# Optimization experiments

Measured on AMD Instinct MI355X. Metric: run time of the kernel, lower is better.

The kernel has to match this reference:

```python
import jax, jax.numpy as jnp
import numpy as np

NUM_RBF = 16
TOP_K = 30
MAX_REL = 32  # max_relative_feature
EPS_D = 1e-6
LN_EPS = 1e-5


def _rbf(D):
    # D: [..., ] -> [..., NUM_RBF]
    mu = jnp.linspace(2.0, 22.0, NUM_RBF)
    sigma = (22.0 - 2.0) / NUM_RBF
    return jnp.exp(-(((D[..., None] - mu) / sigma) ** 2))


def _gather_nb(coords, E_idx):
    # coords: [B,L,3], E_idx: [B,L,K] -> [B,L,K,3]
    return jax.vmap(lambda c, i: c[i])(coords, E_idx)


def reference(X, mask, residue_idx, chain_labels, pe_w, pe_b, edge_w, ln_g, ln_b):
    B, L = X.shape[0], X.shape[1]
    N = X[:, :, 0, :]
    C = X[:, :, 1, :]
    Ca = X[:, :, 2, :]
    O = X[:, :, 3, :]
    # virtual C-beta
    b = Ca - N
    c = C - Ca
    a = jnp.cross(b, c)
    Cb = -0.58273431 * a + 0.56802827 * b - 0.54067466 * c + Ca

    # kNN over masked pairwise C-C distances
    mask2 = mask[:, None, :] * mask[:, :, None]  # [B,L,L]
    dX = C[:, None, :, :] - C[:, :, None, :]
    D = mask2 * jnp.sqrt(jnp.sum(dX ** 2, -1) + EPS_D)
    D_max = jnp.max(D, -1, keepdims=True)
    D_adjust = D + (1.0 - mask2) * D_max
    k = min(TOP_K, L)
    neg_vals, E_idx = jax.lax.top_k(-D_adjust, k)  # smallest distances
    D_neighbors = -neg_vals  # [B,L,K]

    # 25 RBF feature sets: first is the masked topk distance, then 24 atom pairs
    atoms = {'N': N, 'C': C, 'Ca': Ca, 'Cb': Cb, 'O': O}
    pairs = [('N','N'),('Ca','Ca'),('Cb','Cb'),('C','N'),('C','Ca'),('C','Cb'),
             ('N','Ca'),('N','Cb'),('Cb','Ca'),('N','C'),('Ca','C'),('Cb','C'),
             ('Ca','N'),('Cb','N'),('Ca','Cb'),('O','O'),('C','O'),('O','C'),
             ('N','O'),('O','N'),('Cb','O'),('O','Ca'),('O','Cb'),('Ca','O')]
    A_stack = jnp.stack([atoms[p[0]] for p in pairs], 0)  # [P,B,L,3]
    B_stack = jnp.stack([atoms[p[1]] for p in pairs], 0)  # [P,B,L,3]
    Bn = jax.vmap(lambda cb: _gather_nb(cb, E_idx))(B_stack)  # [P,B,L,K,3]
    D_pairs = jnp.sqrt(jnp.sum((A_stack[:, :, :, None, :] - Bn) ** 2, -1) + EPS_D)  # [P,B,L,K]
    RBF_pairs = _rbf(D_pairs)  # [P,B,L,K,R]
    P = len(pairs)
    RBF_pairs = jnp.moveaxis(RBF_pairs, 0, 3).reshape(B, L, k, P * NUM_RBF)
    RBF_all = jnp.concatenate([_rbf(D_neighbors), RBF_pairs], -1)  # [B,L,K,400]

    # positional encodings (relative residue offset gathered at neighbors)
    offset = residue_idx[:, :, None] - residue_idx[:, None, :]  # [B,L,L]
    offset = jnp.take_along_axis(offset, E_idx, axis=2)  # [B,L,K]
    d_chains = (chain_labels[:, :, None] - chain_labels[:, None, :] == 0).astype(jnp.int32)
    E_chains = jnp.take_along_axis(d_chains, E_idx, axis=2)  # [B,L,K]
    d = jnp.clip(offset + MAX_REL, 0, 2 * MAX_REL) * E_chains + (1 - E_chains) * (2 * MAX_REL + 1)
    E_positional = pe_w[d] + pe_b  # one-hot @ W == row gather; [B,L,K,16]

    E = jnp.concatenate([E_positional, RBF_all], -1)  # [B,L,K,416]
    E = E @ edge_w  # [B,L,K,128]
    mu = jnp.mean(E, -1, keepdims=True)
    var = jnp.mean((E - mu) ** 2, -1, keepdims=True)
    E = (E - mu) / jnp.sqrt(var + LN_EPS) * ln_g + ln_b
    return E, E_idx


def setup_inputs() -> dict:
    key = jax.random.key(0)
    ks = jax.random.split(key, 6)
    B, L = 4, 2048
    X = jax.random.normal(ks[0], (B, L, 4, 3), dtype=jnp.float32)
    mask = jnp.ones((B, L), dtype=jnp.float32)
    residue_idx = jnp.arange(B * L, dtype=jnp.int32).reshape(B, L)
    chain_labels = jnp.zeros((B, L), dtype=jnp.int32)
    pe_w = jax.random.normal(ks[1], (66, 16), dtype=jnp.float32) * 0.1
    pe_b = jax.random.normal(ks[2], (16,), dtype=jnp.float32) * 0.1
    edge_w = jax.random.normal(ks[3], (416, 128), dtype=jnp.float32) * 0.05
    ln_g = jnp.ones((128,), dtype=jnp.float32)
    ln_b = jnp.zeros((128,), dtype=jnp.float32)
    return {"X": X, "mask": mask, "residue_idx": residue_idx, "chain_labels": chain_labels,
            "pe_w": pe_w, "pe_b": pe_b, "edge_w": edge_w, "ln_g": ln_g, "ln_b": ln_b}
```

## Files before the change

### kernel.cpp

```cpp
#include <hip/hip_runtime.h>
#include <hip/hip_bf16.h>
#include <cstdint>
#include <cstddef>

#define Bc 4
#define Lc 2048
#define Kc 30
#define Fc 416
#define Nc 128

typedef __bf16 bf16x8 __attribute__((ext_vector_type(8)));
typedef float  f32x4  __attribute__((ext_vector_type(4)));
typedef unsigned short ushortx8 __attribute__((ext_vector_type(8)));

__constant__ int c_pa[24] = {0,2,3,1,1,1,0,0,3,0,2,3,2,3,2,4,1,4,0,4,3,4,4,2};
__constant__ int c_pb[24] = {0,2,3,0,2,3,2,3,2,1,1,1,0,0,3,4,4,1,4,0,4,2,3,2};

__device__ __forceinline__ unsigned long long u64min(unsigned long long a, unsigned long long b) {
    return a < b ? a : b;
}
__device__ __forceinline__ unsigned long long u64max(unsigned long long a, unsigned long long b) {
    return a > b ? a : b;
}

__device__ __forceinline__ unsigned short f2bf(float f) {
    __hip_bfloat16 h = __float2bfloat16(f);
    return *(unsigned short*)&h;
}

__device__ __forceinline__ void rbf8(float d, float mu0, float* v) {
    const float u0 = (d - mu0) * 0.8f;
    v[0] = __expf(-u0 * u0);
    float rr = __expf(fmaf(2.1333333f, u0, -1.1377778f));
    #pragma unroll
    for (int m = 1; m < 8; ++m) {
        v[m] = v[m - 1] * rr;
        rr *= 0.10274083f;
    }
}

template<int CTRL>
__device__ __forceinline__ float dpp_radd(float x) {
    const int r = __builtin_amdgcn_update_dpp(0, __float_as_int(x), CTRL, 0xf, 0xf, true);
    return x + __int_as_float(r);
}
__device__ __forceinline__ float row16_sum(float x) {
    x = dpp_radd<0x121>(x);
    x = dpp_radd<0x122>(x);
    x = dpp_radd<0x124>(x);
    x = dpp_radd<0x128>(x);
    return x;
}

__global__ __launch_bounds__(256) void prep_all(const float* __restrict__ Wg,
                                                const float* __restrict__ X,
                                                const float* __restrict__ mask,
                                                unsigned short* __restrict__ Wt,
                                                float4* __restrict__ Cpk) {
    const int blk = blockIdx.x;
    if (blk < 208) {
        const int id = blk * 256 + threadIdx.x;
        const int n = id / Fc, k = id - n * Fc;
        Wt[id] = f2bf(Wg[k * Nc + n]);
    } else {
        const int id = (blk - 208) * 256 + threadIdx.x;
        float4 o;
        o.x = X[(size_t)id * 12 + 3];
        o.y = X[(size_t)id * 12 + 4];
        o.z = X[(size_t)id * 12 + 5];
        o.w = mask[id];
        Cpk[id] = o;
    }
}

__global__ __launch_bounds__(256) void topk3(
    const float4* __restrict__ Cpk,
    int* __restrict__ eidx, float* __restrict__ dnb, float* __restrict__ outEidx)
{
#pragma clang fp contract(off)
    __shared__ unsigned long long pairs[4][256];
    __shared__ int scnt[4];
    const int t = threadIdx.x;
    const int lane = t & 63, wv = t >> 6;
    const int row = blockIdx.x * 4 + wv;

    if (lane == 0) scnt[wv] = 0;

    const float4 ci = Cpk[row];
    const float cix = ci.x, ciy = ci.y, ciz = ci.z, mi = ci.w;
    const float4* base = Cpk + (row & ~(Lc - 1));

    float D[32], am[32];
    float dmax = -1e30f;
    #pragma unroll 8
    for (int s = 0; s < 32; ++s) {
        const float4 f4 = base[s * 64 + lane];
        const float dx = f4.x - cix;
        const float dy = f4.y - ciy;
        const float dz = f4.z - ciz;
        const float ss = dx * dx + dy * dy + dz * dz;
        const float dist = sqrtf(ss + 1e-6f);
        const float m2 = mi * f4.w;
        D[s] = m2 * dist;
        am[s] = 1.0f - m2;
        dmax = fmaxf(dmax, D[s]);
    }
    #pragma unroll
    for (int off = 32; off; off >>= 1) dmax = fmaxf(dmax, __shfl_xor(dmax, off, 64));

    unsigned uv[32];
    unsigned long long lmin = ~0ULL;
    #pragma unroll 8
    for (int s = 0; s < 32; ++s) {
        const float Dadj = D[s] + am[s] * dmax;
        uv[s] = __float_as_uint(Dadj);
        const unsigned long long k =
            ((unsigned long long)uv[s] << 32) | (unsigned)(s * 64 + lane);
        lmin = u64min(lmin, k);
    }

    unsigned long long sv = lmin;
    #pragma unroll
    for (int k = 2; k <= 64; k <<= 1) {
        #pragma unroll
        for (int j = k >> 1; j > 0; j >>= 1) {
            const unsigned long long o =
                (unsigned long long)__shfl_xor((long long)sv, j, 64);
            const bool takeMin = (((lane & k) == 0) == ((lane & j) == 0));
            sv = takeMin ? u64min(sv, o) : u64max(sv, o);
        }
    }
    const unsigned long long Tkey =
        (unsigned long long)__shfl((long long)sv, 29, 64);

    #pragma unroll 8
    for (int s = 0; s < 32; ++s) {
        const unsigned long long key =
            ((unsigned long long)uv[s] << 32) | (unsigned)(s * 64 + lane);
        if (key <= Tkey) {
            const int pos = atomicAdd(&scnt[wv], 1);
            if (pos < 256) pairs[wv][pos] = key;
        }
    }
    const int S = min(scnt[wv], 256);

    for (int p = lane; p < S; p += 64) {
        const unsigned long long kp = pairs[wv][p];
        int r = 0;
        for (int q = 0; q < S; ++q)
            r += (pairs[wv][q] < kp) ? 1 : 0;
        if (r < Kc) {
            const int j = (int)(kp & 0xffffffffULL);
            eidx[row * Kc + r] = j;
            dnb[row * Kc + r] = __uint_as_float((unsigned)(kp >> 32));
            outEidx[(size_t)row * Kc + r] = (float)j;
        }
    }
}

__global__ __launch_bounds__(512, 4) void edge_mfma5(
    const float* __restrict__ X, const int* __restrict__ ridx, const int* __restrict__ clab,
    const float* __restrict__ pe_w, const float* __restrict__ pe_b,
    const unsigned short* __restrict__ Wt,
    const float* __restrict__ ln_g, const float* __restrict__ ln_b,
    const int* __restrict__ eidx, const float* __restrict__ dnb,
    float* __restrict__ outE)
{
    __shared__ unsigned short Bs[2][8][512];
    __shared__ float atomsA[4][17];
    __shared__ float atomsB[120][17];
    __shared__ float dnb_s[120];
    __shared__ int   pid_s[120];

    const int blk = blockIdx.x;
    const int t   = threadIdx.x;
    const int lane = t & 63, wv = t >> 6;
    const int b   = blk >> 9;
    const int cl  = lane & 15, q = lane >> 4;

    if (t < 124) {
        int j;
        float* dst;
        if (t < 120) {
            j = eidx[(blk * 4 + t / 30) * Kc + (t % 30)];
            dst = &atomsB[t][0];
            dnb_s[t] = dnb[(blk * 4 + t / 30) * Kc + (t % 30)];
            const int rowi = blk * 4 + t / 30;
            const int jg = b * Lc + j;
            const int off = ridx[rowi] - ridx[jg];
            const int ec  = (clab[rowi] == clab[jg]) ? 1 : 0;
            pid_s[t] = ec ? min(max(off + 32, 0), 64) : 65;
        } else {
            j = (blk * 4 + (t - 120)) & (Lc - 1);
            dst = &atomsA[t - 120][0];
        }
        const float* p = X + (size_t)(b * Lc + j) * 12;
        const float Nx = p[0],  Ny = p[1],  Nz = p[2];
        const float Cx = p[3],  Cy = p[4],  Cz = p[5];
        const float Cax = p[6], Cay = p[7], Caz = p[8];
        const float Ox = p[9],  Oy = p[10], Oz = p[11];
        const float bx = Cax - Nx, by = Cay - Ny, bz = Caz - Nz;
        const float cx = Cx - Cax, cy = Cy - Cay, cz = Cz - Caz;
        const float ax = by * cz - bz * cy;
        const float ay = bz * cx - bx * cz;
        const float az = bx * cy - by * cx;
        dst[0] = Nx;  dst[1] = Ny;  dst[2] = Nz;
        dst[3] = Cx;  dst[4] = Cy;  dst[5] = Cz;
        dst[6] = Cax; dst[7] = Cay; dst[8] = Caz;
        dst[9]  = -0.58273431f * ax + 0.56802827f * bx - 0.54067466f * cx + Cax;
        dst[10] = -0.58273431f * ay + 0.56802827f * by - 0.54067466f * cy + Cay;
        dst[11] = -0.58273431f * az + 0.56802827f * bz - 0.54067466f * cz + Caz;
        dst[12] = Ox; dst[13] = Oy; dst[14] = Oz;
    }

    const unsigned short* gW = Wt + (wv * 16 + cl) * Fc + q * 8;
    {
        *(ushortx8*)&Bs[0][wv][lane * 8] = *(const ushortx8*)gW;
    }
    __syncthreads();

    f32x4 acc[8];
    #pragma unroll
    for (int n = 0; n < 8; ++n) acc[n] = (f32x4){0.f, 0.f, 0.f, 0.f};

    const int row0 = wv * 16 + cl;
    const int e0 = min(row0, 119);
    const int r0 = e0 / 30;

    auto afrag = [&](int kc) -> bf16x8 {
        float v[8];
        if (kc == 0) {
            if (q < 2) {
                const int base = pid_s[e0] * 16 + q * 8;
                const float4 p0 = *(const float4*)&pe_w[base];
                const float4 p1 = *(const float4*)&pe_w[base + 4];
                const float4 b0 = *(const float4*)&pe_b[q * 8];
                const float4 b1 = *(const float4*)&pe_b[q * 8 + 4];
                v[0] = p0.x + b0.x; v[1] = p0.y + b0.y;
                v[2] = p0.z + b0.z; v[3] = p0.w + b0.w;
                v[4] = p1.x + b1.x; v[5] = p1.y + b1.y;
                v[6] = p1.z + b1.z; v[7] = p1.w + b1.w;
            } else {
                rbf8(dnb_s[e0], (q == 2) ? 2.0f : 12.6666667f, v);
            }
        } else {
            const int p  = 2 * kc - 2 + (q >> 1);
            const int a_ = c_pa[p], b_ = c_pb[p];
            const float dx = atomsA[r0][a_ * 3 + 0] - atomsB[e0][b_ * 3 + 0];
            const float dy = atomsA[r0][a_ * 3 + 1] - atomsB[e0][b_ * 3 + 1];
            const float dz = atomsA[r0][a_ * 3 + 2] - atomsB[e0][b_ * 3 + 2];
            const float d = sqrtf(dx * dx + dy * dy + dz * dz + 1e-6f);
            rbf8(d, (q & 1) ? 12.6666667f : 2.0f, v);
        }
        ushortx8 o;
        #pragma unroll
        for (int m = 0; m < 8; ++m) o[m] = f2bf(v[m]);
        return __builtin_bit_cast(bf16x8, o);
    };

    bf16x8 a0c = afrag(0);

    for (int kc = 0; kc < 13; ++kc) {
        const int cur = kc & 1;
        ushortx8 st;
        bf16x8 a0n;
        if (kc < 12) {
            st = *(const ushortx8*)(gW + (kc + 1) * 32);
            a0n = afrag(kc + 1);
        }
        #pragma unroll
        for (int n = 0; n < 8; ++n) {
            const bf16x8 bb = __builtin_bit_cast(bf16x8,
                *(const ushortx8*)&Bs[cur][n][lane * 8]);
            acc[n] = __builtin_amdgcn_mfma_f32_16x16x32_bf16(a0c, bb, acc[n], 0, 0, 0);
        }
        if (kc < 12) {
            *(ushortx8*)&Bs[cur ^ 1][wv][lane * 8] = st;
        }
        __syncthreads();
        a0c = a0n;
    }

    float gcol[8], bcol[8];
    #pragma unroll
    for (int n = 0; n < 8; ++n) {
        gcol[n] = ln_g[n * 16 + cl];
        bcol[n] = ln_b[n * 16 + cl];
    }
    #pragma unroll
    for (int reg = 0; reg < 4; ++reg) {
        const int rl = wv * 16 + q * 4 + reg;
        float s1 = 0.f, s2 = 0.f;
        #pragma unroll
        for (int n = 0; n < 8; ++n) {
            const float v = acc[n][reg];
            s1 += v; s2 += v * v;
        }
        s1 = row16_sum(s1);
        s2 = row16_sum(s2);
        if (rl < 120) {
            const float mu = s1 * (1.0f / 128.0f);
            const float var = s2 * (1.0f / 128.0f) - mu * mu;
            const float rstd = rsqrtf(var + 1e-5f);
            const size_t base = ((size_t)(blk * 120 + rl)) * 128 + cl;
            #pragma unroll
            for (int n = 0; n < 8; ++n) {
                outE[base + n * 16] =
                    (acc[n][reg] - mu) * rstd * gcol[n] + bcol[n];
            }
        }
    }
}

extern "C" void kernel_launch(void* const* d_in, const int* in_sizes, int n_in,
                              void* d_out, int out_size, void* d_ws, size_t ws_size,
                              hipStream_t stream) {
    const float* X     = (const float*)d_in[0];
    const float* mask  = (const float*)d_in[1];
    const int*   ridx  = (const int*)d_in[2];
    const int*   clab  = (const int*)d_in[3];
    const float* pe_w  = (const float*)d_in[4];
    const float* pe_b  = (const float*)d_in[5];
    const float* edge_w = (const float*)d_in[6];
    const float* ln_g  = (const float*)d_in[7];
    const float* ln_b  = (const float*)d_in[8];

    float* outE   = (float*)d_out;
    float* outIdx = outE + (size_t)Bc * Lc * Kc * Nc;

    char* ws = (char*)d_ws;
    int*   eidx = (int*)ws;
    float* dnbw = (float*)(ws + 983040);
    unsigned short* Wt = (unsigned short*)(ws + 1966080);
    float4* Cpk = (float4*)(ws + 2072576);

    prep_all<<<240, 256, 0, stream>>>(edge_w, X, mask, Wt, Cpk);
    topk3<<<Bc * Lc / 4, 256, 0, stream>>>(Cpk, eidx, dnbw, outIdx);
    edge_mfma5<<<Bc * Lc / 4, 512, 0, stream>>>(X, ridx, clab, pe_w, pe_b, Wt,
                                                ln_g, ln_b, eidx, dnbw, outE);
}
```

Baseline: 102.7 us.

## Make edge kernel persistent with full weight matrix resident in LDS

The edge MFMA kernel now runs as a persistent grid of 256 blocks, each handling 8 tiles of 4 rows. It loads the whole bf16 weight matrix (13x8x512 halfwords) into shared memory once and reuses it across the tiles, so the per-k-chunk double-buffered weight streaming and its barriers inside the k loop go away. In exchange the block uses about 106KB of LDS, which lowers occupancy to roughly one block per CU. Only 256 blocks are launched, and the serial per-tile atom gather with its barriers is no longer overlapped by other resident blocks.

```diff
diff --git a/kernel.cpp b/kernel.cpp
--- a/kernel.cpp
+++ b/kernel.cpp
@@ -158,7 +158,7 @@
     }
 }
 
-__global__ __launch_bounds__(512, 4) void edge_mfma5(
+__global__ __launch_bounds__(512) void edge_mfma6(
     const float* __restrict__ X, const int* __restrict__ ridx, const int* __restrict__ clab,
     const float* __restrict__ pe_w, const float* __restrict__ pe_b,
     const unsigned short* __restrict__ Wt,
@@ -166,119 +166,21 @@
     const int* __restrict__ eidx, const float* __restrict__ dnb,
     float* __restrict__ outE)
 {
-    __shared__ unsigned short Bs[2][8][512];
+    __shared__ unsigned short Wl[13][8][512];
     __shared__ float atomsA[4][17];
     __shared__ float atomsB[120][17];
     __shared__ float dnb_s[120];
     __shared__ int   pid_s[120];
 
-    const int blk = blockIdx.x;
-    const int t   = threadIdx.x;
+    const int t = threadIdx.x;
     const int lane = t & 63, wv = t >> 6;
-    const int b   = blk >> 9;
     const int cl  = lane & 15, q = lane >> 4;
 
-    if (t < 124) {
-        int j;
-        float* dst;
-        if (t < 120) {
-            j = eidx[(blk * 4 + t / 30) * Kc + (t % 30)];
-            dst = &atomsB[t][0];
-            dnb_s[t] = dnb[(blk * 4 + t / 30) * Kc + (t % 30)];
-            const int rowi = blk * 4 + t / 30;
-            const int jg = b * Lc + j;
-            const int off = ridx[rowi] - ridx[jg];
-            const int ec  = (clab[rowi] == clab[jg]) ? 1 : 0;
-            pid_s[t] = ec ? min(max(off + 32, 0), 64) : 65;
-        } else {
-            j = (blk * 4 + (t - 120)) & (Lc - 1);
-            dst = &atomsA[t - 120][0];
-        }
-        const float* p = X + (size_t)(b * Lc + j) * 12;
-        const float Nx = p[0],  Ny = p[1],  Nz = p[2];
-        const float Cx = p[3],  Cy = p[4],  Cz = p[5];
-        const float Cax = p[6], Cay = p[7], Caz = p[8];
-        const float Ox = p[9],  Oy = p[10], Oz = p[11];
-        const float bx = Cax - Nx, by = Cay - Ny, bz = Caz - Nz;
-        const float cx = Cx - Cax, cy = Cy - Cay, cz = Cz - Caz;
-        const float ax = by * cz - bz * cy;
-        const float ay = bz * cx - bx * cz;
-        const float az = bx * cy - by * cx;
-        dst[0] = Nx;  dst[1] = Ny;  dst[2] = Nz;
-        dst[3] = Cx;  dst[4] = Cy;  dst[5] = Cz;
-        dst[6] = Cax; dst[7] = Cay; dst[8] = Caz;
-        dst[9]  = -0.58273431f * ax + 0.56802827f * bx - 0.54067466f * cx + Cax;
-        dst[10] = -0.58273431f * ay + 0.56802827f * by - 0.54067466f * cy + Cay;
-        dst[11] = -0.58273431f * az + 0.56802827f * bz - 0.54067466f * cz + Caz;
-        dst[12] = Ox; dst[13] = Oy; dst[14] = Oz;
-    }
-
-    const unsigned short* gW = Wt + (wv * 16 + cl) * Fc + q * 8;
     {
-        *(ushortx8*)&Bs[0][wv][lane * 8] = *(const ushortx8*)gW;
-    }
-    __syncthreads();
-
-    f32x4 acc[8];
-    #pragma unroll
-    for (int n = 0; n < 8; ++n) acc[n] = (f32x4){0.f, 0.f, 0.f, 0.f};
-
-    const int row0 = wv * 16 + cl;
-    const int e0 = min(row0, 119);
-    const int r0 = e0 / 30;
-
-    auto afrag = [&](int kc) -> bf16x8 {
-        float v[8];
-        if (kc == 0) {
-            if (q < 2) {
-                const int base = pid_s[e0] * 16 + q * 8;
-                const float4 p0 = *(const float4*)&pe_w[base];
-                const float4 p1 = *(const float4*)&pe_w[base + 4];
-                const float4 b0 = *(const float4*)&pe_b[q * 8];
-                const float4 b1 = *(const float4*)&pe_b[q * 8 + 4];
-                v[0] = p0.x + b0.x; v[1] = p0.y + b0.y;
-                v[2] = p0.z + b0.z; v[3] = p0.w + b0.w;
-                v[4] = p1.x + b1.x; v[5] = p1.y + b1.y;
-                v[6] = p1.z + b1.z; v[7] = p1.w + b1.w;
-            } else {
-                rbf8(dnb_s[e0], (q == 2) ? 2.0f : 12.6666667f, v);
-            }
-        } else {
-            const int p  = 2 * kc - 2 + (q >> 1);
-            const int a_ = c_pa[p], b_ = c_pb[p];
-            const float dx = atomsA[r0][a_ * 3 + 0] - atomsB[e0][b_ * 3 + 0];
-            const float dy = atomsA[r0][a_ * 3 + 1] - atomsB[e0][b_ * 3 + 1];
-            const float dz = atomsA[r0][a_ * 3 + 2] - atomsB[e0][b_ * 3 + 2];
-            const float d = sqrtf(dx * dx + dy * dy + dz * dz + 1e-6f);
-            rbf8(d, (q & 1) ? 12.6666667f : 2.0f, v);
-        }
-        ushortx8 o;
+        const unsigned short* gW = Wt + (wv * 16 + cl) * Fc + q * 8;
         #pragma unroll
-        for (int m = 0; m < 8; ++m) o[m] = f2bf(v[m]);
-        return __builtin_bit_cast(bf16x8, o);
-    };
-
-    bf16x8 a0c = afrag(0);
-
-    for (int kc = 0; kc < 13; ++kc) {
-        const int cur = kc & 1;
-        ushortx8 st;
-        bf16x8 a0n;
-        if (kc < 12) {
-            st = *(const ushortx8*)(gW + (kc + 1) * 32);
-            a0n = afrag(kc + 1);
-        }
-        #pragma unroll
-        for (int n = 0; n < 8; ++n) {
-            const bf16x8 bb = __builtin_bit_cast(bf16x8,
-                *(const ushortx8*)&Bs[cur][n][lane * 8]);
-            acc[n] = __builtin_amdgcn_mfma_f32_16x16x32_bf16(a0c, bb, acc[n], 0, 0, 0);
-        }
-        if (kc < 12) {
-            *(ushortx8*)&Bs[cur ^ 1][wv][lane * 8] = st;
-        }
-        __syncthreads();
-        a0c = a0n;
+        for (int kc = 0; kc < 13; ++kc)
+            *(ushortx8*)&Wl[kc][wv][lane * 8] = *(const ushortx8*)(gW + kc * 32);
     }
 
     float gcol[8], bcol[8];
@@ -287,26 +189,122 @@
         gcol[n] = ln_g[n * 16 + cl];
         bcol[n] = ln_b[n * 16 + cl];
     }
-    #pragma unroll
-    for (int reg = 0; reg < 4; ++reg) {
-        const int rl = wv * 16 + q * 4 + reg;
-        float s1 = 0.f, s2 = 0.f;
+
+    const int row0 = wv * 16 + cl;
+    const int e0 = min(row0, 119);
+    const int r0 = e0 / 30;
+
+    for (int g = 0; g < 8; ++g) {
+        const int tile = blockIdx.x * 8 + g;
+        const int b    = tile >> 9;
+
+        __syncthreads();
+
+        if (t < 124) {
+            int j;
+            float* dst;
+            if (t < 120) {
+                j = eidx[(tile * 4 + t / 30) * Kc + (t % 30)];
+                dst = &atomsB[t][0];
+                dnb_s[t] = dnb[(tile * 4 + t / 30) * Kc + (t % 30)];
+                const int rowi = tile * 4 + t / 30;
+                const int jg = b * Lc + j;
+                const int off = ridx[rowi] - ridx[jg];
+                const int ec  = (clab[rowi] == clab[jg]) ? 1 : 0;
+                pid_s[t] = ec ? min(max(off + 32, 0), 64) : 65;
+            } else {
+                j = (tile * 4 + (t - 120)) & (Lc - 1);
+                dst = &atomsA[t - 120][0];
+            }
+            const float* p = X + (size_t)(b * Lc + j) * 12;
+            const float Nx = p[0],  Ny = p[1],  Nz = p[2];
+            const float Cx = p[3],  Cy = p[4],  Cz = p[5];
+            const float Cax = p[6], Cay = p[7], Caz = p[8];
+            const float Ox = p[9],  Oy = p[10], Oz = p[11];
+            const float bx = Cax - Nx, by = Cay - Ny, bz = Caz - Nz;
+            const float cx = Cx - Cax, cy = Cy - Cay, cz = Cz - Caz;
+            const float ax = by * cz - bz * cy;
+            const float ay = bz * cx - bx * cz;
+            const float az = bx * cy - by * cx;
+            dst[0] = Nx;  dst[1] = Ny;  dst[2] = Nz;
+            dst[3] = Cx;  dst[4] = Cy;  dst[5] = Cz;
+            dst[6] = Cax; dst[7] = Cay; dst[8] = Caz;
+            dst[9]  = -0.58273431f * ax + 0.56802827f * bx - 0.54067466f * cx + Cax;
+            dst[10] = -0.58273431f * ay + 0.56802827f * by - 0.54067466f * cy + Cay;
+            dst[11] = -0.58273431f * az + 0.56802827f * bz - 0.54067466f * cz + Caz;
+            dst[12] = Ox; dst[13] = Oy; dst[14] = Oz;
+        }
+        __syncthreads();
+
+        f32x4 acc[8];
         #pragma unroll
-        for (int n = 0; n < 8; ++n) {
-            const float v = acc[n][reg];
-            s1 += v; s2 += v * v;
-        }
-        s1 = row16_sum(s1);
-        s2 = row16_sum(s2);
-        if (rl < 120) {
-            const float mu = s1 * (1.0f / 128.0f);
-            const float var = s2 * (1.0f / 128.0f) - mu * mu;
-            const float rstd = rsqrtf(var + 1e-5f);
-            const size_t base = ((size_t)(blk * 120 + rl)) * 128 + cl;
+        for (int n = 0; n < 8; ++n) acc[n] = (f32x4){0.f, 0.f, 0.f, 0.f};
+
+        auto afrag = [&](int kc) -> bf16x8 {
+            float v[8];
+            if (kc == 0) {
+                if (q < 2) {
+                    const int base = pid_s[e0] * 16 + q * 8;
+                    const float4 p0 = *(const float4*)&pe_w[base];
+                    const float4 p1 = *(const float4*)&pe_w[base + 4];
+                    const float4 b0 = *(const float4*)&pe_b[q * 8];
+                    const float4 b1 = *(const float4*)&pe_b[q * 8 + 4];
+                    v[0] = p0.x + b0.x; v[1] = p0.y + b0.y;
+                    v[2] = p0.z + b0.z; v[3] = p0.w + b0.w;
+                    v[4] = p1.x + b1.x; v[5] = p1.y + b1.y;
+                    v[6] = p1.z + b1.z; v[7] = p1.w + b1.w;
+                } else {
+                    rbf8(dnb_s[e0], (q == 2) ? 2.0f : 12.6666667f, v);
+                }
+            } else {
+                const int p  = 2 * kc - 2 + (q >> 1);
+                const int a_ = c_pa[p], b_ = c_pb[p];
+                const float dx = atomsA[r0][a_ * 3 + 0] - atomsB[e0][b_ * 3 + 0];
+                const float dy = atomsA[r0][a_ * 3 + 1] - atomsB[e0][b_ * 3 + 1];
+                const float dz = atomsA[r0][a_ * 3 + 2] - atomsB[e0][b_ * 3 + 2];
+                const float d = sqrtf(dx * dx + dy * dy + dz * dz + 1e-6f);
+                rbf8(d, (q & 1) ? 12.6666667f : 2.0f, v);
+            }
+            ushortx8 o;
+            #pragma unroll
+            for (int m = 0; m < 8; ++m) o[m] = f2bf(v[m]);
+            return __builtin_bit_cast(bf16x8, o);
+        };
+
+        bf16x8 a0c = afrag(0);
+        for (int kc = 0; kc < 13; ++kc) {
+            bf16x8 a0n;
+            if (kc < 12) a0n = afrag(kc + 1);
             #pragma unroll
             for (int n = 0; n < 8; ++n) {
-                outE[base + n * 16] =
-                    (acc[n][reg] - mu) * rstd * gcol[n] + bcol[n];
+                const bf16x8 bb = __builtin_bit_cast(bf16x8,
+                    *(const ushortx8*)&Wl[kc][n][lane * 8]);
+                acc[n] = __builtin_amdgcn_mfma_f32_16x16x32_bf16(a0c, bb, acc[n], 0, 0, 0);
+            }
+            a0c = a0n;
+        }
+
+        #pragma unroll
+        for (int reg = 0; reg < 4; ++reg) {
+            const int rl = wv * 16 + q * 4 + reg;
+            float s1 = 0.f, s2 = 0.f;
+            #pragma unroll
+            for (int n = 0; n < 8; ++n) {
+                const float v = acc[n][reg];
+                s1 += v; s2 += v * v;
+            }
+            s1 = row16_sum(s1);
+            s2 = row16_sum(s2);
+            if (rl < 120) {
+                const float mu = s1 * (1.0f / 128.0f);
+                const float var = s2 * (1.0f / 128.0f) - mu * mu;
+                const float rstd = rsqrtf(var + 1e-5f);
+                const size_t base = ((size_t)(tile * 120 + rl)) * 128 + cl;
+                #pragma unroll
+                for (int n = 0; n < 8; ++n) {
+                    outE[base + n * 16] =
+                        (acc[n][reg] - mu) * rstd * gcol[n] + bcol[n];
+                }
             }
         }
     }
@@ -336,6 +334,6 @@
 
     prep_all<<<240, 256, 0, stream>>>(edge_w, X, mask, Wt, Cpk);
     topk3<<<Bc * Lc / 4, 256, 0, stream>>>(Cpk, eidx, dnbw, outIdx);
-    edge_mfma5<<<Bc * Lc / 4, 512, 0, stream>>>(X, ridx, clab, pe_w, pe_b, Wt,
-                                                ln_g, ln_b, eidx, dnbw, outE);
-}
+    edge_mfma6<<<256, 512, 0, stream>>>(X, ridx, clab, pe_w, pe_b, Wt,
+                                        ln_g, ln_b, eidx, dnbw, outE);
+}
```

Result: slower. 108.8 us (+6.0%).
